# Kernel tuning notes

Hardware: AMD Instinct MI355X
Metric: run time of the kernel (lower is better)

The kernel has to match this reference:

```python
import jax, jax.numpy as jnp
import numpy as np

CELL = 1024
IN = 1024
HYB = 1024
SPK = 256
B = 8192

def setup_inputs() -> dict:
    key = jax.random.key(0)
    ks = jax.random.split(key, 13)
    s = lambda fan: 1.0 / np.sqrt(fan)
    return {
        "x": jax.random.normal(ks[0], (B, IN), jnp.float32),
        "ctm": jax.random.normal(ks[1], (B, CELL), jnp.float32),
        "htm": jax.random.normal(ks[2], (B, CELL), jnp.float32),
        "ztm": jax.random.normal(ks[3], (B, HYB), jnp.float32),
        "speaker_affine": jax.random.normal(ks[4], (B, SPK), jnp.float32),
        "Ww": jax.random.uniform(ks[5], (IN, 4 * CELL), jnp.float32, -s(IN), s(IN)),
        "Wb": jax.random.uniform(ks[6], (4 * CELL,), jnp.float32, -s(IN), s(IN)),
        "Uw": jax.random.uniform(ks[7], (CELL, 4 * CELL), jnp.float32, -s(CELL), s(CELL)),
        "Ub": jax.random.uniform(ks[8], (4 * CELL,), jnp.float32, -s(CELL), s(CELL)),
        "Vw": jax.random.uniform(ks[9], (HYB, CELL), jnp.float32, -s(HYB), s(HYB)),
        "Vb": jax.random.uniform(ks[10], (CELL,), jnp.float32, -s(HYB), s(HYB)),
        "Sw": jax.random.uniform(ks[11], (SPK, 4 * CELL), jnp.float32, -s(SPK), s(SPK)),
        "Sb": jax.random.uniform(ks[12], (4 * CELL,), jnp.float32, -s(SPK), s(SPK)),
    }

def reference(x, ctm, htm, ztm, speaker_affine, Ww, Wb, Uw, Ub, Vw, Vb, Sw, Sb):
    # sums: [B, 4*CELL] = W(x) + U(htm) + S(speaker)
    sums = (x @ Ww + Wb) + (htm @ Uw + Ub) + (speaker_affine @ Sw + Sb)
    hybrid = ztm @ Vw + Vb  # [B, CELL]
    f_t = jax.nn.sigmoid(sums[:, :CELL])
    i_t = jax.nn.sigmoid(sums[:, CELL:2 * CELL])
    o_t = jax.nn.sigmoid(sums[:, 2 * CELL:3 * CELL])
    ch_t = jnp.tanh(sums[:, 3 * CELL:])
    f_t_ = jax.nn.sigmoid(hybrid)
    c_t = f_t * ctm + i_t * ch_t + f_t_ * ctm
    h_t = jnp.tanh(c_t) * o_t
    return (c_t, h_t)
```

## Files before the change

### kernel.cpp

```cpp
#include <hip/hip_runtime.h>

#define B_DIM 8192
#define CELL  1024
#define KA    3328
#define BM    256
#define BN    256
#define BK    64

typedef unsigned short u16;
typedef __attribute__((ext_vector_type(8))) short bf16x8;
typedef __attribute__((ext_vector_type(4))) float f32x4;
typedef __attribute__((ext_vector_type(4))) float fx4;
typedef __attribute__((ext_vector_type(4))) unsigned short u16x4;

__device__ inline u16 f2bf(float f) {
  unsigned u = __float_as_uint(f);
  return (u16)((u + 0x7FFFu + ((u >> 16) & 1u)) >> 16);
}
__device__ inline float sigmoidf(float v) { return 1.0f / (1.0f + __expf(-v)); }

__global__ void cvt_cat(const float* __restrict__ src, u16* __restrict__ dst,
                        int shift, int colOff, int n4) {
  int i = blockIdx.x * 256 + threadIdx.x;
  if (i >= n4) return;
  int e = i << 2;
  int row = e >> shift;
  int col = e & ((1 << shift) - 1);
  float4 v = *reinterpret_cast<const float4*>(src + e);
  u16x4 o;
  o[0] = f2bf(v.x); o[1] = f2bf(v.y); o[2] = f2bf(v.z); o[3] = f2bf(v.w);
  *reinterpret_cast<u16x4*>(dst + (size_t)row * KA + colOff + col) = o;
}

__global__ void wtrans(const float* __restrict__ src, int N,
                       u16* __restrict__ dst, int KT, int koff, int packed) {
  __shared__ float tile[32][33];
  int n0 = blockIdx.x * 32, k0 = blockIdx.y * 32;
  int tx = threadIdx.x, ty = threadIdx.y;
#pragma unroll
  for (int j = 0; j < 4; ++j)
    tile[ty + j * 8][tx] = src[(size_t)(k0 + ty + j * 8) * N + n0 + tx];
  __syncthreads();
#pragma unroll
  for (int j = 0; j < 4; ++j) {
    int jj = n0 + ty + j * 8;
    int p = packed ? (((jj & 1023) >> 4) << 6) + ((jj >> 10) << 4) + (jj & 15) : jj;
    dst[(size_t)p * KT + koff + k0 + tx] = f2bf(tile[tx][ty + j * 8]);
  }
}

__device__ __forceinline__ void gload_lds16(const void* g, void* l) {
  __builtin_amdgcn_global_load_lds((const __attribute__((address_space(1))) void*)g,
                                   (__attribute__((address_space(3))) void*)l,
                                   16, 0, 0);
}

__device__ __forceinline__ void stage_half(const u16* __restrict__ g0, int ldk,
                                           u16* ldsTile, int half, int kt,
                                           int wave, int lane) {
#pragma unroll
  for (int k2 = 0; k2 < 2; ++k2) {
    const int r0 = half * 128 + k2 * 64 + wave * 8;
    const int r = r0 + (lane >> 3);
    const int slot = (lane & 7) ^ (lane >> 3);
    const u16* g = g0 + (size_t)r * ldk + kt * 64 + slot * 8;
    gload_lds16((const void*)g, (void*)(ldsTile + r0 * 64));
  }
}

#define LD_A(ASP, QP)                                                              \
  aq[0][0] = *reinterpret_cast<const bf16x8*>((ASP) + aBase0 + (2 * (QP)) * 1024);     \
  aq[0][1] = *reinterpret_cast<const bf16x8*>((ASP) + aBase1 + (2 * (QP)) * 1024);     \
  aq[1][0] = *reinterpret_cast<const bf16x8*>((ASP) + aBase0 + (2 * (QP) + 1) * 1024); \
  aq[1][1] = *reinterpret_cast<const bf16x8*>((ASP) + aBase1 + (2 * (QP) + 1) * 1024);

#define LD_B(BSP)                                                                  \
  _Pragma("unroll")                                                                \
  for (int n = 0; n < 4; ++n) {                                                    \
    br[n][0] = *reinterpret_cast<const bf16x8*>((BSP) + bBase0 + n * 1024);        \
    br[n][1] = *reinterpret_cast<const bf16x8*>((BSP) + bBase1 + n * 1024);        \
  }

#define MFMA_PH(QP)                                                                \
  __builtin_amdgcn_s_setprio(1);                                                   \
  _Pragma("unroll")                                                                \
  for (int q = 0; q < 2; ++q) {                                                    \
    _Pragma("unroll")                                                              \
    for (int n = 0; n < 4; ++n) {                                                  \
      acc[2 * (QP) + q][n] = __builtin_amdgcn_mfma_f32_16x16x32_bf16(              \
          aq[q][0], br[n][0], acc[2 * (QP) + q][n], 0, 0, 0);                      \
      acc[2 * (QP) + q][n] = __builtin_amdgcn_mfma_f32_16x16x32_bf16(              \
          aq[q][1], br[n][1], acc[2 * (QP) + q][n], 0, 0, 0);                      \
    }                                                                              \
  }                                                                                \
  __builtin_amdgcn_s_setprio(0);

#define ENTRY_BAR                                                                  \
  __builtin_amdgcn_sched_barrier(0);                                               \
  __builtin_amdgcn_s_barrier();                                                    \
  asm volatile("s_waitcnt lgkmcnt(0)" ::: "memory");                               \
  __builtin_amdgcn_sched_barrier(0);

#define EXIT_BAR __builtin_amdgcn_s_barrier();

__global__ __launch_bounds__(512, 2) void gemm_fused(
    const u16* __restrict__ Afull, const u16* __restrict__ WT4p,
    const u16* __restrict__ VwT, const float* __restrict__ ctm,
    const float* __restrict__ Wb, const float* __restrict__ Ub,
    const float* __restrict__ Sb, const float* __restrict__ Vb,
    float* __restrict__ outC, float* __restrict__ outH) {
  __shared__ u16 As[2][BM * BK];
  __shared__ u16 Bs[2][BN * BK];
  const int tid = threadIdx.x;
  const int wave = tid >> 6, lane = tid & 63;
  const int wm = wave >> 2, wn = wave & 3;
  const int lrow = lane & 15, khi = lane >> 4;

  const int bid = blockIdx.x;
  const int tilei = ((bid & 7) << 6) | (bid >> 3);
  const int nb = tilei >> 5, mb = tilei & 31;
  const int m0 = mb * 256;
  const u16* Ag = Afull + (size_t)m0 * KA;
  const u16* Ah = Afull + (size_t)m0 * KA + 2304;
  const u16* Bg = WT4p + (size_t)(nb * 256) * 2304;

  const int sw = lane & 7;
  const int swz0 = ((0 + khi) ^ sw) * 8;
  const int swz1 = ((4 + khi) ^ sw) * 8;
  const int aBase0 = (wm * 128 + lrow) * 64 + swz0;
  const int aBase1 = (wm * 128 + lrow) * 64 + swz1;
  const int bBase0 = (wn * 64 + lrow) * 64 + swz0;
  const int bBase1 = (wn * 64 + lrow) * 64 + swz1;

  const int co = nb * 64 + wn * 16 + lrow;
  const u16* HgRow = VwT + (size_t)co * 1024;

  f32x4 acc[8][4];
#pragma unroll
  for (int m2 = 0; m2 < 8; ++m2)
#pragma unroll
    for (int n2 = 0; n2 < 4; ++n2) acc[m2][n2] = (f32x4){0.f, 0.f, 0.f, 0.f};
  bf16x8 aq[2][2], br[4][2];
  u16* As0 = As[0]; u16* As1 = As[1]; u16* Bs0 = Bs[0]; u16* Bs1 = Bs[1];

  stage_half(Ag, KA, As0, 0, 0, wave, lane);
  stage_half(Ag, KA, As0, 1, 0, wave, lane);
  stage_half(Bg, 2304, Bs0, 0, 0, wave, lane);
  stage_half(Bg, 2304, Bs0, 1, 0, wave, lane);
  stage_half(Bg, 2304, Bs1, 0, 1, wave, lane);
  stage_half(Bg, 2304, Bs1, 1, 1, wave, lane);
  asm volatile("s_waitcnt vmcnt(4)" ::: "memory");
  __builtin_amdgcn_s_barrier();

#pragma unroll 1
  for (int it = 0; it < 18; ++it) {
    const int t = it * 2;
    const bool nl = (t + 2 < 36);
    LD_B(Bs0)
    LD_A(As0, 0)
    stage_half(Ag, KA, As1, 0, t + 1, wave, lane);
    ENTRY_BAR MFMA_PH(0) EXIT_BAR

    LD_A(As0, 1)
    stage_half(Ag, KA, As1, 1, t + 1, wave, lane);
    ENTRY_BAR MFMA_PH(1) EXIT_BAR

    LD_A(As0, 2)
    if (nl) stage_half(Bg, 2304, Bs0, 0, t + 2, wave, lane);
    ENTRY_BAR MFMA_PH(2) EXIT_BAR

    LD_A(As0, 3)
    if (nl) stage_half(Bg, 2304, Bs0, 1, t + 2, wave, lane);
    ENTRY_BAR MFMA_PH(3)
    if (nl) { asm volatile("s_waitcnt vmcnt(4)" ::: "memory"); }
    else    { asm volatile("s_waitcnt vmcnt(0)" ::: "memory"); }
    EXIT_BAR

    LD_B(Bs1)
    LD_A(As1, 0)
    if (nl) stage_half(Ag, KA, As0, 0, t + 2, wave, lane);
    ENTRY_BAR MFMA_PH(0) EXIT_BAR

    LD_A(As1, 1)
    if (nl) stage_half(Ag, KA, As0, 1, t + 2, wave, lane);
    ENTRY_BAR MFMA_PH(1) EXIT_BAR

    LD_A(As1, 2)
    if (nl) stage_half(Bg, 2304, Bs1, 0, t + 3, wave, lane);
    ENTRY_BAR MFMA_PH(2) EXIT_BAR

    LD_A(As1, 3)
    if (nl) stage_half(Bg, 2304, Bs1, 1, t + 3, wave, lane);
    ENTRY_BAR MFMA_PH(3)
    if (nl) { asm volatile("s_waitcnt vmcnt(4)" ::: "memory"); }
    else    { asm volatile("s_waitcnt vmcnt(0)" ::: "memory"); }
    EXIT_BAR
  }

  f32x4 acch[8];
#pragma unroll
  for (int m2 = 0; m2 < 8; ++m2) acch[m2] = (f32x4){0.f, 0.f, 0.f, 0.f};

#pragma unroll 1
  for (int kt = 0; kt < 16; ++kt) {
    __syncthreads();
    stage_half(Ah, KA, As0, 0, kt, wave, lane);
    stage_half(Ah, KA, As0, 1, kt, wave, lane);
    __syncthreads();
    bf16x8 bh0 = *reinterpret_cast<const bf16x8*>(HgRow + kt * 64 + khi * 8);
    bf16x8 bh1 = *reinterpret_cast<const bf16x8*>(HgRow + kt * 64 + 32 + khi * 8);
#pragma unroll
    for (int qp = 0; qp < 4; ++qp) {
      LD_A(As0, qp)
      acch[2 * qp]     = __builtin_amdgcn_mfma_f32_16x16x32_bf16(aq[0][0], bh0, acch[2 * qp], 0, 0, 0);
      acch[2 * qp]     = __builtin_amdgcn_mfma_f32_16x16x32_bf16(aq[0][1], bh1, acch[2 * qp], 0, 0, 0);
      acch[2 * qp + 1] = __builtin_amdgcn_mfma_f32_16x16x32_bf16(aq[1][0], bh0, acch[2 * qp + 1], 0, 0, 0);
      acch[2 * qp + 1] = __builtin_amdgcn_mfma_f32_16x16x32_bf16(aq[1][1], bh1, acch[2 * qp + 1], 0, 0, 0);
    }
  }

  const float bf = Wb[co] + Ub[co] + Sb[co];
  const float bi = Wb[1024 + co] + Ub[1024 + co] + Sb[1024 + co];
  const float bo = Wb[2048 + co] + Ub[2048 + co] + Sb[2048 + co];
  const float bc = Wb[3072 + co] + Ub[3072 + co] + Sb[3072 + co];
  const float bv = Vb[co];
#pragma unroll
  for (int mf = 0; mf < 8; ++mf) {
    const int r0 = m0 + wm * 128 + mf * 16 + khi * 4;
#pragma unroll
    for (int j = 0; j < 4; ++j) {
      const size_t idx = (size_t)(r0 + j) * CELL + co;
      float f_ = sigmoidf(acc[mf][0][j] + bf);
      float i_ = sigmoidf(acc[mf][1][j] + bi);
      float o_ = sigmoidf(acc[mf][2][j] + bo);
      float g_ = tanhf(acc[mf][3][j] + bc);
      float fh = sigmoidf(acch[mf][j] + bv);
      float ct = ctm[idx];
      float cc = (f_ + fh) * ct + i_ * g_;
      outC[idx] = cc;
      outH[idx] = tanhf(cc) * o_;
    }
  }
}

extern "C" void kernel_launch(void* const* d_in, const int* in_sizes, int n_in,
                              void* d_out, int out_size, void* d_ws, size_t ws_size,
                              hipStream_t stream) {
  const float* x   = (const float*)d_in[0];
  const float* ctm = (const float*)d_in[1];
  const float* htm = (const float*)d_in[2];
  const float* ztm = (const float*)d_in[3];
  const float* spk = (const float*)d_in[4];
  const float* Ww  = (const float*)d_in[5];
  const float* Wb  = (const float*)d_in[6];
  const float* Uw  = (const float*)d_in[7];
  const float* Ub  = (const float*)d_in[8];
  const float* Vw  = (const float*)d_in[9];
  const float* Vb  = (const float*)d_in[10];
  const float* Sw  = (const float*)d_in[11];
  const float* Sb  = (const float*)d_in[12];

  u16* Afull = (u16*)d_ws;
  u16* WT4p  = Afull + (size_t)B_DIM * KA;
  u16* VwT   = WT4p + (size_t)4096 * 2304;
  float* outC = (float*)d_out;
  float* outH = outC + (size_t)B_DIM * CELL;

  cvt_cat<<<8192, 256, 0, stream>>>(x,   Afull, 10, 0,    2097152);
  cvt_cat<<<8192, 256, 0, stream>>>(htm, Afull, 10, 1024, 2097152);
  cvt_cat<<<2048, 256, 0, stream>>>(spk, Afull, 8,  2048, 524288);
  cvt_cat<<<8192, 256, 0, stream>>>(ztm, Afull, 10, 2304, 2097152);

  wtrans<<<dim3(128, 32), dim3(32, 8), 0, stream>>>(Ww, 4096, WT4p, 2304, 0,    1);
  wtrans<<<dim3(128, 32), dim3(32, 8), 0, stream>>>(Uw, 4096, WT4p, 2304, 1024, 1);
  wtrans<<<dim3(128, 8),  dim3(32, 8), 0, stream>>>(Sw, 4096, WT4p, 2304, 2048, 1);
  wtrans<<<dim3(32, 32),  dim3(32, 8), 0, stream>>>(Vw, 1024, VwT,  1024, 0,    0);

  gemm_fused<<<512, 512, 0, stream>>>(Afull, WT4p, VwT, ctm, Wb, Ub, Sb, Vb, outC, outH);
}
```

Measured before the change: 295.1 us.

## Triple-buffer A tiles, double-buffer hybrid loop, fuse conversions, fast activations

Expands the A shared-memory buffers to three so A tiles are prefetched two K-steps ahead, with the main loop rewritten as a six-tile rotation and a deeper vmcnt wait. The hybrid Vw loop now double-buffers its A tiles instead of staging synchronously with two barriers per step. The four input conversion launches are merged into one kernel, and sigmoid/tanh use hardware reciprocal approximations. This raises LDS use to 160KB per block and slightly lowers activation precision.

```diff
diff --git a/kernel.cpp b/kernel.cpp
--- a/kernel.cpp
+++ b/kernel.cpp
@@ -17,12 +17,23 @@
   unsigned u = __float_as_uint(f);
   return (u16)((u + 0x7FFFu + ((u >> 16) & 1u)) >> 16);
 }
-__device__ inline float sigmoidf(float v) { return 1.0f / (1.0f + __expf(-v)); }
-
-__global__ void cvt_cat(const float* __restrict__ src, u16* __restrict__ dst,
-                        int shift, int colOff, int n4) {
-  int i = blockIdx.x * 256 + threadIdx.x;
-  if (i >= n4) return;
+__device__ inline float rcp_f(float x) { return __builtin_amdgcn_rcpf(x); }
+__device__ inline float sigmoid_f(float v) { return rcp_f(1.0f + __expf(-v)); }
+__device__ inline float tanh_f(float v) {
+  float e = __expf(2.0f * v);
+  return 1.0f - 2.0f * rcp_f(e + 1.0f);
+}
+
+__global__ void cvt_all(const float* __restrict__ x, const float* __restrict__ htm,
+                        const float* __restrict__ spk, const float* __restrict__ ztm,
+                        u16* __restrict__ dst) {
+  int b = blockIdx.x;
+  const float* src; int shift, colOff, base;
+  if (b < 8192)       { src = x;   shift = 10; colOff = 0;    base = 0; }
+  else if (b < 16384) { src = htm; shift = 10; colOff = 1024; base = 8192; }
+  else if (b < 18432) { src = spk; shift = 8;  colOff = 2048; base = 16384; }
+  else                { src = ztm; shift = 10; colOff = 2304; base = 18432; }
+  int i = (b - base) * 256 + threadIdx.x;
   int e = i << 2;
   int row = e >> shift;
   int col = e & ((1 << shift) - 1);
@@ -103,13 +114,35 @@
 
 #define EXIT_BAR __builtin_amdgcn_s_barrier();
 
+#define TILE6(Acur, Bcur, An2, Bn2, TT)                                            \
+  {                                                                                \
+    const int t2 = (TT) + 2;                                                       \
+    const bool nl = (t2 < 36);                                                     \
+    LD_B(Bcur)                                                                     \
+    LD_A(Acur, 0)                                                                  \
+    if (nl) stage_half(Ag, KA, An2, 0, t2, wave, lane);                            \
+    ENTRY_BAR MFMA_PH(0) EXIT_BAR                                                  \
+    LD_A(Acur, 1)                                                                  \
+    if (nl) stage_half(Ag, KA, An2, 1, t2, wave, lane);                            \
+    ENTRY_BAR MFMA_PH(1) EXIT_BAR                                                  \
+    LD_A(Acur, 2)                                                                  \
+    if (nl) stage_half(Bg, 2304, Bn2, 0, t2, wave, lane);                          \
+    ENTRY_BAR MFMA_PH(2) EXIT_BAR                                                  \
+    LD_A(Acur, 3)                                                                  \
+    if (nl) stage_half(Bg, 2304, Bn2, 1, t2, wave, lane);                          \
+    ENTRY_BAR MFMA_PH(3)                                                           \
+    if (nl) { asm volatile("s_waitcnt vmcnt(8)" ::: "memory"); }                   \
+    else    { asm volatile("s_waitcnt vmcnt(0)" ::: "memory"); }                   \
+    EXIT_BAR                                                                       \
+  }
+
 __global__ __launch_bounds__(512, 2) void gemm_fused(
     const u16* __restrict__ Afull, const u16* __restrict__ WT4p,
     const u16* __restrict__ VwT, const float* __restrict__ ctm,
     const float* __restrict__ Wb, const float* __restrict__ Ub,
     const float* __restrict__ Sb, const float* __restrict__ Vb,
     float* __restrict__ outC, float* __restrict__ outH) {
-  __shared__ u16 As[2][BM * BK];
+  __shared__ u16 As[3][BM * BK];
   __shared__ u16 Bs[2][BN * BK];
   const int tid = threadIdx.x;
   const int wave = tid >> 6, lane = tid & 63;
@@ -141,77 +174,51 @@
 #pragma unroll
     for (int n2 = 0; n2 < 4; ++n2) acc[m2][n2] = (f32x4){0.f, 0.f, 0.f, 0.f};
   bf16x8 aq[2][2], br[4][2];
-  u16* As0 = As[0]; u16* As1 = As[1]; u16* Bs0 = Bs[0]; u16* Bs1 = Bs[1];
+  u16* As0 = As[0]; u16* As1 = As[1]; u16* As2 = As[2];
+  u16* Bs0 = Bs[0]; u16* Bs1 = Bs[1];
 
   stage_half(Ag, KA, As0, 0, 0, wave, lane);
   stage_half(Ag, KA, As0, 1, 0, wave, lane);
   stage_half(Bg, 2304, Bs0, 0, 0, wave, lane);
   stage_half(Bg, 2304, Bs0, 1, 0, wave, lane);
+  stage_half(Ag, KA, As1, 0, 1, wave, lane);
+  stage_half(Ag, KA, As1, 1, 1, wave, lane);
   stage_half(Bg, 2304, Bs1, 0, 1, wave, lane);
   stage_half(Bg, 2304, Bs1, 1, 1, wave, lane);
-  asm volatile("s_waitcnt vmcnt(4)" ::: "memory");
+  asm volatile("s_waitcnt vmcnt(8)" ::: "memory");
   __builtin_amdgcn_s_barrier();
 
 #pragma unroll 1
-  for (int it = 0; it < 18; ++it) {
-    const int t = it * 2;
-    const bool nl = (t + 2 < 36);
-    LD_B(Bs0)
-    LD_A(As0, 0)
-    stage_half(Ag, KA, As1, 0, t + 1, wave, lane);
-    ENTRY_BAR MFMA_PH(0) EXIT_BAR
-
-    LD_A(As0, 1)
-    stage_half(Ag, KA, As1, 1, t + 1, wave, lane);
-    ENTRY_BAR MFMA_PH(1) EXIT_BAR
-
-    LD_A(As0, 2)
-    if (nl) stage_half(Bg, 2304, Bs0, 0, t + 2, wave, lane);
-    ENTRY_BAR MFMA_PH(2) EXIT_BAR
-
-    LD_A(As0, 3)
-    if (nl) stage_half(Bg, 2304, Bs0, 1, t + 2, wave, lane);
-    ENTRY_BAR MFMA_PH(3)
-    if (nl) { asm volatile("s_waitcnt vmcnt(4)" ::: "memory"); }
-    else    { asm volatile("s_waitcnt vmcnt(0)" ::: "memory"); }
-    EXIT_BAR
-
-    LD_B(Bs1)
-    LD_A(As1, 0)
-    if (nl) stage_half(Ag, KA, As0, 0, t + 2, wave, lane);
-    ENTRY_BAR MFMA_PH(0) EXIT_BAR
-
-    LD_A(As1, 1)
-    if (nl) stage_half(Ag, KA, As0, 1, t + 2, wave, lane);
-    ENTRY_BAR MFMA_PH(1) EXIT_BAR
-
-    LD_A(As1, 2)
-    if (nl) stage_half(Bg, 2304, Bs1, 0, t + 3, wave, lane);
-    ENTRY_BAR MFMA_PH(2) EXIT_BAR
-
-    LD_A(As1, 3)
-    if (nl) stage_half(Bg, 2304, Bs1, 1, t + 3, wave, lane);
-    ENTRY_BAR MFMA_PH(3)
-    if (nl) { asm volatile("s_waitcnt vmcnt(4)" ::: "memory"); }
-    else    { asm volatile("s_waitcnt vmcnt(0)" ::: "memory"); }
-    EXIT_BAR
+  for (int tb = 0; tb < 36; tb += 6) {
+    TILE6(As0, Bs0, As2, Bs0, tb + 0)
+    TILE6(As1, Bs1, As0, Bs1, tb + 1)
+    TILE6(As2, Bs0, As1, Bs0, tb + 2)
+    TILE6(As0, Bs1, As2, Bs1, tb + 3)
+    TILE6(As1, Bs0, As0, Bs0, tb + 4)
+    TILE6(As2, Bs1, As1, Bs1, tb + 5)
   }
 
   f32x4 acch[8];
 #pragma unroll
   for (int m2 = 0; m2 < 8; ++m2) acch[m2] = (f32x4){0.f, 0.f, 0.f, 0.f};
+
+  stage_half(Ah, KA, As0, 0, 0, wave, lane);
+  stage_half(Ah, KA, As0, 1, 0, wave, lane);
 
 #pragma unroll 1
   for (int kt = 0; kt < 16; ++kt) {
     __syncthreads();
-    stage_half(Ah, KA, As0, 0, kt, wave, lane);
-    stage_half(Ah, KA, As0, 1, kt, wave, lane);
-    __syncthreads();
+    u16* AsP = (kt & 1) ? As1 : As0;
+    if (kt + 1 < 16) {
+      u16* AsN = (kt & 1) ? As0 : As1;
+      stage_half(Ah, KA, AsN, 0, kt + 1, wave, lane);
+      stage_half(Ah, KA, AsN, 1, kt + 1, wave, lane);
+    }
     bf16x8 bh0 = *reinterpret_cast<const bf16x8*>(HgRow + kt * 64 + khi * 8);
     bf16x8 bh1 = *reinterpret_cast<const bf16x8*>(HgRow + kt * 64 + 32 + khi * 8);
 #pragma unroll
     for (int qp = 0; qp < 4; ++qp) {
-      LD_A(As0, qp)
+      LD_A(AsP, qp)
       acch[2 * qp]     = __builtin_amdgcn_mfma_f32_16x16x32_bf16(aq[0][0], bh0, acch[2 * qp], 0, 0, 0);
       acch[2 * qp]     = __builtin_amdgcn_mfma_f32_16x16x32_bf16(aq[0][1], bh1, acch[2 * qp], 0, 0, 0);
       acch[2 * qp + 1] = __builtin_amdgcn_mfma_f32_16x16x32_bf16(aq[1][0], bh0, acch[2 * qp + 1], 0, 0, 0);
@@ -230,15 +237,15 @@
 #pragma unroll
     for (int j = 0; j < 4; ++j) {
       const size_t idx = (size_t)(r0 + j) * CELL + co;
-      float f_ = sigmoidf(acc[mf][0][j] + bf);
-      float i_ = sigmoidf(acc[mf][1][j] + bi);
-      float o_ = sigmoidf(acc[mf][2][j] + bo);
-      float g_ = tanhf(acc[mf][3][j] + bc);
-      float fh = sigmoidf(acch[mf][j] + bv);
+      float f_ = sigmoid_f(acc[mf][0][j] + bf);
+      float i_ = sigmoid_f(acc[mf][1][j] + bi);
+      float o_ = sigmoid_f(acc[mf][2][j] + bo);
+      float g_ = tanh_f(acc[mf][3][j] + bc);
+      float fh = sigmoid_f(acch[mf][j] + bv);
       float ct = ctm[idx];
       float cc = (f_ + fh) * ct + i_ * g_;
       outC[idx] = cc;
-      outH[idx] = tanhf(cc) * o_;
+      outH[idx] = tanh_f(cc) * o_;
     }
   }
 }
@@ -266,10 +273,7 @@
   float* outC = (float*)d_out;
   float* outH = outC + (size_t)B_DIM * CELL;
 
-  cvt_cat<<<8192, 256, 0, stream>>>(x,   Afull, 10, 0,    2097152);
-  cvt_cat<<<8192, 256, 0, stream>>>(htm, Afull, 10, 1024, 2097152);
-  cvt_cat<<<2048, 256, 0, stream>>>(spk, Afull, 8,  2048, 524288);
-  cvt_cat<<<8192, 256, 0, stream>>>(ztm, Afull, 10, 2304, 2097152);
+  cvt_all<<<26624, 256, 0, stream>>>(x, htm, spk, ztm, Afull);
 
   wtrans<<<dim3(128, 32), dim3(32, 8), 0, stream>>>(Ww, 4096, WT4p, 2304, 0,    1);
   wtrans<<<dim3(128, 32), dim3(32, 8), 0, stream>>>(Uw, 4096, WT4p, 2304, 1024, 1);
```

Result: slower. 390.5 us (+32.3%).

## Fuse input conversions, double-buffer hybrid GEMM A tiles, use fast activations

Applied to the files above, without the earlier changes.

The four input-conversion launches are merged into one kernel that picks its source by block index, which removes launch overhead. The hybrid (Vw) GEMM loop now double-buffers its A tile between As0 and As1, prefetching the next k-tile while computing the current one, and drops one barrier per iteration. The epilogue's sigmoid and tanh use hardware reciprocal plus exp in place of division and tanhf. Risks are a race if As1 is still in use or the single remaining barrier is not enough, and small accuracy loss in tanh for large inputs.

```diff
diff --git a/kernel.cpp b/kernel.cpp
--- a/kernel.cpp
+++ b/kernel.cpp
@@ -17,12 +17,23 @@
   unsigned u = __float_as_uint(f);
   return (u16)((u + 0x7FFFu + ((u >> 16) & 1u)) >> 16);
 }
-__device__ inline float sigmoidf(float v) { return 1.0f / (1.0f + __expf(-v)); }
-
-__global__ void cvt_cat(const float* __restrict__ src, u16* __restrict__ dst,
-                        int shift, int colOff, int n4) {
-  int i = blockIdx.x * 256 + threadIdx.x;
-  if (i >= n4) return;
+__device__ inline float rcp_f(float x) { return __builtin_amdgcn_rcpf(x); }
+__device__ inline float sigmoid_f(float v) { return rcp_f(1.0f + __expf(-v)); }
+__device__ inline float tanh_f(float v) {
+  float e = __expf(2.0f * v);
+  return 1.0f - 2.0f * rcp_f(e + 1.0f);
+}
+
+__global__ void cvt_all(const float* __restrict__ x, const float* __restrict__ htm,
+                        const float* __restrict__ spk, const float* __restrict__ ztm,
+                        u16* __restrict__ dst) {
+  int b = blockIdx.x;
+  const float* src; int shift, colOff, base;
+  if (b < 8192)       { src = x;   shift = 10; colOff = 0;    base = 0; }
+  else if (b < 16384) { src = htm; shift = 10; colOff = 1024; base = 8192; }
+  else if (b < 18432) { src = spk; shift = 8;  colOff = 2048; base = 16384; }
+  else                { src = ztm; shift = 10; colOff = 2304; base = 18432; }
+  int i = (b - base) * 256 + threadIdx.x;
   int e = i << 2;
   int row = e >> shift;
   int col = e & ((1 << shift) - 1);
@@ -201,17 +212,23 @@
 #pragma unroll
   for (int m2 = 0; m2 < 8; ++m2) acch[m2] = (f32x4){0.f, 0.f, 0.f, 0.f};
 
+  stage_half(Ah, KA, As0, 0, 0, wave, lane);
+  stage_half(Ah, KA, As0, 1, 0, wave, lane);
+
 #pragma unroll 1
   for (int kt = 0; kt < 16; ++kt) {
     __syncthreads();
-    stage_half(Ah, KA, As0, 0, kt, wave, lane);
-    stage_half(Ah, KA, As0, 1, kt, wave, lane);
-    __syncthreads();
+    u16* AsP = (kt & 1) ? As1 : As0;
+    if (kt + 1 < 16) {
+      u16* AsN = (kt & 1) ? As0 : As1;
+      stage_half(Ah, KA, AsN, 0, kt + 1, wave, lane);
+      stage_half(Ah, KA, AsN, 1, kt + 1, wave, lane);
+    }
     bf16x8 bh0 = *reinterpret_cast<const bf16x8*>(HgRow + kt * 64 + khi * 8);
     bf16x8 bh1 = *reinterpret_cast<const bf16x8*>(HgRow + kt * 64 + 32 + khi * 8);
 #pragma unroll
     for (int qp = 0; qp < 4; ++qp) {
-      LD_A(As0, qp)
+      LD_A(AsP, qp)
       acch[2 * qp]     = __builtin_amdgcn_mfma_f32_16x16x32_bf16(aq[0][0], bh0, acch[2 * qp], 0, 0, 0);
       acch[2 * qp]     = __builtin_amdgcn_mfma_f32_16x16x32_bf16(aq[0][1], bh1, acch[2 * qp], 0, 0, 0);
       acch[2 * qp + 1] = __builtin_amdgcn_mfma_f32_16x16x32_bf16(aq[1][0], bh0, acch[2 * qp + 1], 0, 0, 0);
@@ -230,15 +247,15 @@
 #pragma unroll
     for (int j = 0; j < 4; ++j) {
       const size_t idx = (size_t)(r0 + j) * CELL + co;
-      float f_ = sigmoidf(acc[mf][0][j] + bf);
-      float i_ = sigmoidf(acc[mf][1][j] + bi);
-      float o_ = sigmoidf(acc[mf][2][j] + bo);
-      float g_ = tanhf(acc[mf][3][j] + bc);
-      float fh = sigmoidf(acch[mf][j] + bv);
+      float f_ = sigmoid_f(acc[mf][0][j] + bf);
+      float i_ = sigmoid_f(acc[mf][1][j] + bi);
+      float o_ = sigmoid_f(acc[mf][2][j] + bo);
+      float g_ = tanh_f(acc[mf][3][j] + bc);
+      float fh = sigmoid_f(acch[mf][j] + bv);
       float ct = ctm[idx];
       float cc = (f_ + fh) * ct + i_ * g_;
       outC[idx] = cc;
-      outH[idx] = tanhf(cc) * o_;
+      outH[idx] = tanh_f(cc) * o_;
     }
   }
 }
@@ -266,10 +283,7 @@
   float* outC = (float*)d_out;
   float* outH = outC + (size_t)B_DIM * CELL;
 
-  cvt_cat<<<8192, 256, 0, stream>>>(x,   Afull, 10, 0,    2097152);
-  cvt_cat<<<8192, 256, 0, stream>>>(htm, Afull, 10, 1024, 2097152);
-  cvt_cat<<<2048, 256, 0, stream>>>(spk, Afull, 8,  2048, 524288);
-  cvt_cat<<<8192, 256, 0, stream>>>(ztm, Afull, 10, 2304, 2097152);
+  cvt_all<<<26624, 256, 0, stream>>>(x, htm, spk, ztm, Afull);
 
   wtrans<<<dim3(128, 32), dim3(32, 8), 0, stream>>>(Ww, 4096, WT4p, 2304, 0,    1);
   wtrans<<<dim3(128, 32), dim3(32, 8), 0, stream>>>(Uw, 4096, WT4p, 2304, 1024, 1);
```

Measured after the change: 254.2 us. -13.8%, faster.
